# Optimization experiments

Hardware: AMD Instinct MI355X
Metric: run time of the kernel (lower is better)

## Reference

```python
import jax, jax.numpy as jnp
import numpy as np

B, SQ, SKV, D = 4, 4096, 4096, 64

def setup_inputs() -> dict:
    key = jax.random.key(0)
    kq, kv = jax.random.split(key)
    query = jax.random.normal(kq, (B, SQ, D), dtype=jnp.float32)
    value = jax.random.normal(kv, (B, SKV, D), dtype=jnp.float32)
    return {"query": query, "value": value}

def reference(query, value):
    # scores = Q @ V^T  (value acts as both keys and values; no 1/sqrt(d) scaling)
    scores = jnp.einsum('bqd,bkd->bqk', query, value)  # [B, SQ, SKV]
    dist = jax.nn.softmax(scores, axis=-1)
    context = jnp.einsum('bqk,bkd->bqd', dist, value)  # [B, SQ, D]
    return context
```

## Files before the change

kernel.cpp:

```cpp
#include <hip/hip_runtime.h>


#define NB   4
#define SQ   4096
#define SKV  4096
#define DH   64
#define L2E  1.44269504088896340736f

typedef _Float16 half8 __attribute__((ext_vector_type(8)));
typedef _Float16 half2v __attribute__((ext_vector_type(2)));
typedef __attribute__((ext_vector_type(4))) float f32x4;
typedef unsigned short u16;

__device__ __forceinline__ u16 f2h(float f) {
  _Float16 h = (_Float16)f;
  return __builtin_bit_cast(u16, h);
}

__global__ __launch_bounds__(256) void prep_kernel(
    const float* __restrict__ V, u16* __restrict__ vh, u16* __restrict__ vt) {
  __shared__ u16 ldsT[16 * 72];
  int blk = blockIdx.x;
  int b   = blk >> 8;
  int rem = blk & 255;
  int j0  = (rem >> 2) << 6;
  int d0  = (rem & 3) << 4;
  int t   = threadIdx.x;
  int j   = t >> 2;
  int dc  = (t & 3) << 2;

  const float* src = V + ((size_t)(b * SKV) + j0 + j) * DH + d0 + dc;
  float4 v4 = *(const float4*)src;
  u16 h[4] = {f2h(v4.x), f2h(v4.y), f2h(v4.z), f2h(v4.w)};
  unsigned p0 = (unsigned)h[0] | ((unsigned)h[1] << 16);
  unsigned p1 = (unsigned)h[2] | ((unsigned)h[3] << 16);
  size_t go = ((size_t)(b * SKV) + j0 + j) * DH + d0 + dc;
  *(uint2*)(vh + go) = make_uint2(p0, p1);

#pragma unroll
  for (int k = 0; k < 4; ++k) ldsT[(dc + k) * 72 + j] = h[k];
  __syncthreads();

  int dl = t >> 4;
  int jc = (t & 15) << 2;
  u16 tr[4];
#pragma unroll
  for (int k = 0; k < 4; ++k) tr[k] = ldsT[dl * 72 + jc + k];
  unsigned q0 = (unsigned)tr[0] | ((unsigned)tr[1] << 16);
  unsigned q1 = (unsigned)tr[2] | ((unsigned)tr[3] << 16);
  *(uint2*)(vt + ((size_t)(b * DH) + d0 + dl) * SKV + j0 + jc) = make_uint2(q0, q1);
}

__global__ __launch_bounds__(256, 4) void attn_kernel(
    const float* __restrict__ Q,
    const u16* __restrict__ vh,
    const u16* __restrict__ vt,
    u16* __restrict__ po,
    float* __restrict__ pm,
    float* __restrict__ pl,
    int S, int kvLen) {
  __shared__ __align__(16) u16 s_v[64 * 72];
  __shared__ __align__(16) u16 s_vt[64 * 72];
  __shared__ __align__(16) u16 s_pt[8][64 * 20];

  int blk  = blockIdx.x;
  int tile = blk / S;
  int s    = blk - tile * S;
  int b    = tile >> 5;
  int q0   = (tile & 31) << 7;
  int kv0  = s * kvLen;
  int t    = threadIdx.x;
  int wave = t >> 6;
  int lane = t & 63;
  int col  = lane & 15;
  int quad = lane >> 4;
  int qw   = q0 + (wave << 5);

  half8 qf[2][2];
#pragma unroll
  for (int set = 0; set < 2; ++set) {
#pragma unroll
    for (int kc = 0; kc < 2; ++kc) {
      const float* qp = Q + ((size_t)(b * SQ) + qw + set * 16 + col) * DH +
                        kc * 32 + (quad << 3);
      float4 a0 = *(const float4*)qp;
      float4 a1 = *(const float4*)(qp + 4);
      half8 h;
      h[0] = (_Float16)(a0.x * L2E); h[1] = (_Float16)(a0.y * L2E);
      h[2] = (_Float16)(a0.z * L2E); h[3] = (_Float16)(a0.w * L2E);
      h[4] = (_Float16)(a1.x * L2E); h[5] = (_Float16)(a1.y * L2E);
      h[6] = (_Float16)(a1.z * L2E); h[7] = (_Float16)(a1.w * L2E);
      qf[set][kc] = h;
    }
  }

  f32x4 o[2][4];
  float m_r[2][4], l_r[2][4];
#pragma unroll
  for (int set = 0; set < 2; ++set)
#pragma unroll
    for (int nf = 0; nf < 4; ++nf) {
      o[set][nf] = (f32x4){0.f, 0.f, 0.f, 0.f};
      m_r[set][nf] = -1e30f;
      l_r[set][nf] = 0.f;
    }

  int sr = t >> 2;
  int sc = (t & 3) << 4;
  const u16* gv  = vh + (size_t)(b * SKV) * DH;
  const u16* gvt = vt + (size_t)(b * DH) * SKV;

  for (int j0 = kv0; j0 < kv0 + kvLen; j0 += 64) {
    __syncthreads();
    {
      size_t g = (size_t)(j0 + sr) * DH + sc;
      uint4 a0 = *(const uint4*)(gv + g);
      uint4 a1 = *(const uint4*)(gv + g + 8);
      size_t gt = (size_t)sr * SKV + j0 + sc;
      uint4 c0 = *(const uint4*)(gvt + gt);
      uint4 c1 = *(const uint4*)(gvt + gt + 8);
      int l0 = sr * 72 + sc;
      *(uint4*)(s_v + l0)      = a0;
      *(uint4*)(s_v + l0 + 8)  = a1;
      *(uint4*)(s_vt + l0)     = c0;
      *(uint4*)(s_vt + l0 + 8) = c1;
    }
    __syncthreads();

    f32x4 sf[2][4];
#pragma unroll
    for (int set = 0; set < 2; ++set)
#pragma unroll
      for (int nf = 0; nf < 4; ++nf) sf[set][nf] = (f32x4){0.f, 0.f, 0.f, 0.f};
#pragma unroll
    for (int nf = 0; nf < 4; ++nf) {
#pragma unroll
      for (int kc = 0; kc < 2; ++kc) {
        half8 bv = *(const half8*)(s_v + (nf * 16 + col) * 72 + kc * 32 + (quad << 3));
        sf[0][nf] = __builtin_amdgcn_mfma_f32_16x16x32_f16(qf[0][kc], bv, sf[0][nf], 0, 0, 0);
        sf[1][nf] = __builtin_amdgcn_mfma_f32_16x16x32_f16(qf[1][kc], bv, sf[1][nf], 0, 0, 0);
      }
    }

#pragma unroll
    for (int set = 0; set < 2; ++set) {
      float tm[4];
#pragma unroll
      for (int r = 0; r < 4; ++r)
        tm[r] = fmaxf(fmaxf(sf[set][0][r], sf[set][1][r]),
                      fmaxf(sf[set][2][r], sf[set][3][r]));
      half2v h01 = {(_Float16)tm[0], (_Float16)tm[1]};
      half2v h23 = {(_Float16)tm[2], (_Float16)tm[3]};
#pragma unroll
      for (int mask = 1; mask <= 8; mask <<= 1) {
        int i01 = __shfl_xor(__builtin_bit_cast(int, h01), mask, 64);
        int i23 = __shfl_xor(__builtin_bit_cast(int, h23), mask, 64);
        h01 = __builtin_elementwise_max(h01, __builtin_bit_cast(half2v, i01));
        h23 = __builtin_elementwise_max(h23, __builtin_bit_cast(half2v, i23));
      }
      tm[0] = (float)h01[0]; tm[1] = (float)h01[1];
      tm[2] = (float)h23[0]; tm[3] = (float)h23[1];

      float al[4];
#pragma unroll
      for (int r = 0; r < 4; ++r) {
        float mn = fmaxf(m_r[set][r], tm[r]);
        al[r] = exp2f(m_r[set][r] - mn);
        m_r[set][r] = mn;
      }
      float rs[4] = {0.f, 0.f, 0.f, 0.f};
#pragma unroll
      for (int nf = 0; nf < 4; ++nf) {
#pragma unroll
        for (int r = 0; r < 4; ++r) {
          float p = exp2f(sf[set][nf][r] - m_r[set][r]);
          sf[set][nf][r] = p;
          rs[r] += p;
        }
      }
#pragma unroll
      for (int r = 0; r < 4; ++r) l_r[set][r] = l_r[set][r] * al[r] + rs[r];
#pragma unroll
      for (int nf = 0; nf < 4; ++nf)
#pragma unroll
        for (int r = 0; r < 4; ++r) o[set][nf][r] *= al[r];

      u16* pt = &s_pt[wave * 2 + set][0];
#pragma unroll
      for (int nf = 0; nf < 4; ++nf) {
        int j = nf * 16 + col;
        unsigned long long pk =
            (unsigned long long)f2h(sf[set][nf][0]) |
            ((unsigned long long)f2h(sf[set][nf][1]) << 16) |
            ((unsigned long long)f2h(sf[set][nf][2]) << 32) |
            ((unsigned long long)f2h(sf[set][nf][3]) << 48);
        *(unsigned long long*)(pt + j * 20 + (quad << 2)) = pk;
      }
    }

#pragma unroll
    for (int kc = 0; kc < 2; ++kc) {
      half8 pa0, pa1;
      const u16* pt0 = &s_pt[wave * 2 + 0][0];
      const u16* pt1 = &s_pt[wave * 2 + 1][0];
#pragma unroll
      for (int jj = 0; jj < 8; ++jj) {
        int k = kc * 32 + (quad << 3) + jj;
        pa0[jj] = __builtin_bit_cast(_Float16, pt0[k * 20 + col]);
        pa1[jj] = __builtin_bit_cast(_Float16, pt1[k * 20 + col]);
      }
#pragma unroll
      for (int nf = 0; nf < 4; ++nf) {
        half8 bw = *(const half8*)(s_vt + (nf * 16 + col) * 72 + kc * 32 + (quad << 3));
        o[0][nf] = __builtin_amdgcn_mfma_f32_16x16x32_f16(pa0, bw, o[0][nf], 0, 0, 0);
        o[1][nf] = __builtin_amdgcn_mfma_f32_16x16x32_f16(pa1, bw, o[1][nf], 0, 0, 0);
      }
    }
  }

#pragma unroll
  for (int set = 0; set < 2; ++set)
#pragma unroll
    for (int mask = 1; mask <= 8; mask <<= 1)
#pragma unroll
      for (int r = 0; r < 4; ++r)
        l_r[set][r] += __shfl_xor(l_r[set][r], mask, 64);

  int pidx = tile * S + s;
  u16* pob = po + (size_t)pidx * 128 * 64;
#pragma unroll
  for (int set = 0; set < 2; ++set) {
#pragma unroll
    for (int nf = 0; nf < 4; ++nf)
#pragma unroll
      for (int r = 0; r < 4; ++r) {
        int row = (wave << 5) + set * 16 + (quad << 2) + r;
        pob[row * 64 + nf * 16 + col] = f2h(o[set][nf][r]);
      }
  }
  if (col == 0) {
#pragma unroll
    for (int set = 0; set < 2; ++set)
#pragma unroll
      for (int r = 0; r < 4; ++r) {
        int row = (wave << 5) + set * 16 + (quad << 2) + r;
        pm[(size_t)pidx * 128 + row] = m_r[set][r];
        pl[(size_t)pidx * 128 + row] = l_r[set][r];
      }
  }
}

__global__ __launch_bounds__(256) void combine_kernel(
    const u16* __restrict__ po,
    const float* __restrict__ pm,
    const float* __restrict__ pl,
    float* __restrict__ out, int S) {
  int t    = threadIdx.x;
  int rowg = blockIdx.x * 32 + (t >> 3);
  int tile = rowg >> 7;
  int row  = rowg & 127;
  int dc   = (t & 7) << 3;

  float mv[8], lv[8];
  float M = -1e30f;
  for (int s = 0; s < S; ++s) {
    mv[s] = pm[(size_t)(tile * S + s) * 128 + row];
    lv[s] = pl[(size_t)(tile * S + s) * 128 + row];
    M = fmaxf(M, mv[s]);
  }
  float L = 0.f, w[8];
  for (int s = 0; s < S; ++s) {
    w[s] = exp2f(mv[s] - M);
    L += lv[s] * w[s];
  }
  float acc[8] = {0.f, 0.f, 0.f, 0.f, 0.f, 0.f, 0.f, 0.f};
  for (int s = 0; s < S; ++s) {
    const u16* p = po + (size_t)(tile * S + s) * 8192 + row * 64 + dc;
    uint4 raw = *(const uint4*)p;
    half8 x = __builtin_bit_cast(half8, raw);
#pragma unroll
    for (int k = 0; k < 8; ++k) acc[k] += w[s] * (float)x[k];
  }
  float invL = 1.0f / L;
  float* op = out + (size_t)rowg * 64 + dc;
  f32x4 o0 = (f32x4){acc[0], acc[1], acc[2], acc[3]};
  f32x4 o1 = (f32x4){acc[4], acc[5], acc[6], acc[7]};
  *(f32x4*)op       = o0 * invL;
  *(f32x4*)(op + 4) = o1 * invL;
}

extern "C" void kernel_launch(void* const* d_in, const int* in_sizes, int n_in,
                              void* d_out, int out_size, void* d_ws, size_t ws_size,
                              hipStream_t stream) {
  const float* Q = (const float*)d_in[0];
  const float* V = (const float*)d_in[1];
  float* out = (float*)d_out;

  const size_t convBytes = (size_t)2 * NB * SKV * DH * 2;
  auto partBytes = [](int S) {
    return (size_t)NB * 32 * S * ((size_t)128 * 64 * 2 + 128 * 8);
  };
  int S = 8;
  while (S > 1 && ws_size < convBytes + partBytes(S)) S >>= 1;
  int kvLen = SKV / S;

  u16* vh = (u16*)d_ws;
  u16* vt = vh + (size_t)NB * SKV * DH;
  u16* po = vt + (size_t)NB * SKV * DH;
  float* pm = (float*)(po + (size_t)NB * 32 * S * 128 * 64);
  float* pl = pm + (size_t)NB * 32 * S * 128;

  prep_kernel<<<NB * 256, 256, 0, stream>>>(V, vh, vt);
  attn_kernel<<<NB * 32 * S, 256, 0, stream>>>(Q, vh, vt, po, pm, pl, S, kvLen);
  combine_kernel<<<NB * SQ / 32, 256, 0, stream>>>(po, pm, pl, out, S);
}
```

Before: 119.0 us.

## Double-buffer V tiles and keep P in registers via transposed MFMA

Swaps the MFMA operand order so scores come out transposed (query rows along lanes). The softmax max and sum then need only two cross-lane shuffles, and P can feed the second matmul straight from registers through 16x16x16 MFMAs, with no LDS round-trip. V and V^T tiles are double-buffered in LDS with register prefetch, which drops one barrier per iteration. The epilogue stages the output through LDS for coalesced vector stores. The row max is now computed in fp32 instead of fp16, and P is converted with round-toward-zero packing.

```diff
diff --git a/kernel.cpp b/kernel.cpp
--- a/kernel.cpp
+++ b/kernel.cpp
@@ -8,13 +8,20 @@
 #define L2E  1.44269504088896340736f
 
 typedef _Float16 half8 __attribute__((ext_vector_type(8)));
+typedef _Float16 half4 __attribute__((ext_vector_type(4)));
 typedef _Float16 half2v __attribute__((ext_vector_type(2)));
-typedef __attribute__((ext_vector_type(4))) float f32x4;
+typedef float f32x4 __attribute__((ext_vector_type(4)));
 typedef unsigned short u16;
+
+#define MFMA16(a, b, c) __builtin_amdgcn_mfma_f32_16x16x16f16((a), (b), (c), 0, 0, 0)
+#define MFMA32(a, b, c) __builtin_amdgcn_mfma_f32_16x16x32_f16((a), (b), (c), 0, 0, 0)
 
 __device__ __forceinline__ u16 f2h(float f) {
   _Float16 h = (_Float16)f;
   return __builtin_bit_cast(u16, h);
+}
+__device__ __forceinline__ half2v pkrtz(float a, float b) {
+  return __builtin_bit_cast(half2v, __builtin_amdgcn_cvt_pkrtz(a, b));
 }
 
 __global__ __launch_bounds__(256) void prep_kernel(
@@ -59,9 +66,7 @@
     float* __restrict__ pm,
     float* __restrict__ pl,
     int S, int kvLen) {
-  __shared__ __align__(16) u16 s_v[64 * 72];
-  __shared__ __align__(16) u16 s_vt[64 * 72];
-  __shared__ __align__(16) u16 s_pt[8][64 * 20];
+  __shared__ __align__(16) u16 lds[2][2][64 * 72];
 
   int blk  = blockIdx.x;
   int tile = blk / S;
@@ -95,37 +100,46 @@
   }
 
   f32x4 o[2][4];
-  float m_r[2][4], l_r[2][4];
+  float m_r[2] = {-1e30f, -1e30f};
+  float l_r[2] = {0.f, 0.f};
 #pragma unroll
   for (int set = 0; set < 2; ++set)
 #pragma unroll
-    for (int nf = 0; nf < 4; ++nf) {
-      o[set][nf] = (f32x4){0.f, 0.f, 0.f, 0.f};
-      m_r[set][nf] = -1e30f;
-      l_r[set][nf] = 0.f;
-    }
+    for (int nf = 0; nf < 4; ++nf) o[set][nf] = (f32x4){0.f, 0.f, 0.f, 0.f};
 
   int sr = t >> 2;
   int sc = (t & 3) << 4;
   const u16* gv  = vh + (size_t)(b * SKV) * DH;
   const u16* gvt = vt + (size_t)(b * DH) * SKV;
-
-  for (int j0 = kv0; j0 < kv0 + kvLen; j0 += 64) {
+  int l0 = sr * 72 + sc;
+
+  {
+    size_t g  = (size_t)(kv0 + sr) * DH + sc;
+    size_t gt = (size_t)sr * SKV + kv0 + sc;
+    *(uint4*)(&lds[0][0][l0])     = *(const uint4*)(gv + g);
+    *(uint4*)(&lds[0][0][l0 + 8]) = *(const uint4*)(gv + g + 8);
+    *(uint4*)(&lds[0][1][l0])     = *(const uint4*)(gvt + gt);
+    *(uint4*)(&lds[0][1][l0 + 8]) = *(const uint4*)(gvt + gt + 8);
+  }
+
+  int nIter = kvLen >> 6;
+  int cur = 0;
+  for (int it = 0; it < nIter; ++it) {
     __syncthreads();
-    {
-      size_t g = (size_t)(j0 + sr) * DH + sc;
-      uint4 a0 = *(const uint4*)(gv + g);
-      uint4 a1 = *(const uint4*)(gv + g + 8);
+
+    uint4 a0, a1, c0, c1;
+    bool more = (it + 1) < nIter;
+    if (more) {
+      int j0 = kv0 + ((it + 1) << 6);
+      size_t g  = (size_t)(j0 + sr) * DH + sc;
       size_t gt = (size_t)sr * SKV + j0 + sc;
-      uint4 c0 = *(const uint4*)(gvt + gt);
-      uint4 c1 = *(const uint4*)(gvt + gt + 8);
-      int l0 = sr * 72 + sc;
-      *(uint4*)(s_v + l0)      = a0;
-      *(uint4*)(s_v + l0 + 8)  = a1;
-      *(uint4*)(s_vt + l0)     = c0;
-      *(uint4*)(s_vt + l0 + 8) = c1;
-    }
-    __syncthreads();
+      a0 = *(const uint4*)(gv + g);
+      a1 = *(const uint4*)(gv + g + 8);
+      c0 = *(const uint4*)(gvt + gt);
+      c1 = *(const uint4*)(gvt + gt + 8);
+    }
+    const u16* sv  = &lds[cur][0][0];
+    const u16* svt = &lds[cur][1][0];
 
     f32x4 sf[2][4];
 #pragma unroll
@@ -136,117 +150,108 @@
     for (int nf = 0; nf < 4; ++nf) {
 #pragma unroll
       for (int kc = 0; kc < 2; ++kc) {
-        half8 bv = *(const half8*)(s_v + (nf * 16 + col) * 72 + kc * 32 + (quad << 3));
-        sf[0][nf] = __builtin_amdgcn_mfma_f32_16x16x32_f16(qf[0][kc], bv, sf[0][nf], 0, 0, 0);
-        sf[1][nf] = __builtin_amdgcn_mfma_f32_16x16x32_f16(qf[1][kc], bv, sf[1][nf], 0, 0, 0);
+        half8 av = *(const half8*)(sv + (nf * 16 + col) * 72 + kc * 32 + (quad << 3));
+        sf[0][nf] = MFMA32(av, qf[0][kc], sf[0][nf]);
+        sf[1][nf] = MFMA32(av, qf[1][kc], sf[1][nf]);
       }
     }
 
+    half4 pf[2][4];
 #pragma unroll
     for (int set = 0; set < 2; ++set) {
-      float tm[4];
-#pragma unroll
-      for (int r = 0; r < 4; ++r)
-        tm[r] = fmaxf(fmaxf(sf[set][0][r], sf[set][1][r]),
-                      fmaxf(sf[set][2][r], sf[set][3][r]));
-      half2v h01 = {(_Float16)tm[0], (_Float16)tm[1]};
-      half2v h23 = {(_Float16)tm[2], (_Float16)tm[3]};
-#pragma unroll
-      for (int mask = 1; mask <= 8; mask <<= 1) {
-        int i01 = __shfl_xor(__builtin_bit_cast(int, h01), mask, 64);
-        int i23 = __shfl_xor(__builtin_bit_cast(int, h23), mask, 64);
-        h01 = __builtin_elementwise_max(h01, __builtin_bit_cast(half2v, i01));
-        h23 = __builtin_elementwise_max(h23, __builtin_bit_cast(half2v, i23));
+      float tm = sf[set][0][0];
+#pragma unroll
+      for (int nf = 0; nf < 4; ++nf)
+#pragma unroll
+        for (int r = 0; r < 4; ++r) tm = fmaxf(tm, sf[set][nf][r]);
+      tm = fmaxf(tm, __shfl_xor(tm, 16, 64));
+      tm = fmaxf(tm, __shfl_xor(tm, 32, 64));
+      float mn = fmaxf(m_r[set], tm);
+      float al = exp2f(m_r[set] - mn);
+      m_r[set] = mn;
+      float rs = 0.f;
+#pragma unroll
+      for (int nf = 0; nf < 4; ++nf) {
+        float p0 = exp2f(sf[set][nf][0] - mn);
+        float p1 = exp2f(sf[set][nf][1] - mn);
+        float p2 = exp2f(sf[set][nf][2] - mn);
+        float p3 = exp2f(sf[set][nf][3] - mn);
+        rs += (p0 + p1) + (p2 + p3);
+        half2v lo = pkrtz(p0, p1);
+        half2v hi = pkrtz(p2, p3);
+        pf[set][nf] = __builtin_shufflevector(lo, hi, 0, 1, 2, 3);
       }
-      tm[0] = (float)h01[0]; tm[1] = (float)h01[1];
-      tm[2] = (float)h23[0]; tm[3] = (float)h23[1];
-
-      float al[4];
-#pragma unroll
-      for (int r = 0; r < 4; ++r) {
-        float mn = fmaxf(m_r[set][r], tm[r]);
-        al[r] = exp2f(m_r[set][r] - mn);
-        m_r[set][r] = mn;
+      l_r[set] = l_r[set] * al + rs;
+#pragma unroll
+      for (int nf = 0; nf < 4; ++nf)
+#pragma unroll
+        for (int r = 0; r < 4; ++r) o[set][nf][r] *= al;
+    }
+
+#pragma unroll
+    for (int kc4 = 0; kc4 < 4; ++kc4) {
+#pragma unroll
+      for (int nf2 = 0; nf2 < 4; ++nf2) {
+        half4 avt = *(const half4*)(svt + (nf2 * 16 + col) * 72 + kc4 * 16 + (quad << 2));
+        o[0][nf2] = MFMA16(avt, pf[0][kc4], o[0][nf2]);
+        o[1][nf2] = MFMA16(avt, pf[1][kc4], o[1][nf2]);
       }
-      float rs[4] = {0.f, 0.f, 0.f, 0.f};
-#pragma unroll
-      for (int nf = 0; nf < 4; ++nf) {
-#pragma unroll
-        for (int r = 0; r < 4; ++r) {
-          float p = exp2f(sf[set][nf][r] - m_r[set][r]);
-          sf[set][nf][r] = p;
-          rs[r] += p;
-        }
+    }
+
+    if (more) {
+      u16* dv  = &lds[cur ^ 1][0][0];
+      u16* dvt = &lds[cur ^ 1][1][0];
+      *(uint4*)(dv + l0)      = a0;
+      *(uint4*)(dv + l0 + 8)  = a1;
+      *(uint4*)(dvt + l0)     = c0;
+      *(uint4*)(dvt + l0 + 8) = c1;
+    }
+    cur ^= 1;
+  }
+
+#pragma unroll
+  for (int set = 0; set < 2; ++set) {
+    l_r[set] += __shfl_xor(l_r[set], 16, 64);
+    l_r[set] += __shfl_xor(l_r[set], 32, 64);
+  }
+  int pidx = tile * S + s;
+  if (quad == 0) {
+#pragma unroll
+    for (int set = 0; set < 2; ++set) {
+      int row = (wave << 5) + set * 16 + col;
+      pm[(size_t)pidx * 128 + row] = m_r[set];
+      pl[(size_t)pidx * 128 + row] = l_r[set];
+    }
+  }
+
+  __syncthreads();
+  u16* tp = &lds[0][0][0];
+#pragma unroll
+  for (int set = 0; set < 2; ++set) {
+    int q = (wave << 5) + set * 16 + col;
+#pragma unroll
+    for (int nf2 = 0; nf2 < 4; ++nf2) {
+#pragma unroll
+      for (int r2 = 0; r2 < 4; r2 += 2) {
+        unsigned pk = (unsigned)f2h(o[set][nf2][r2]) |
+                      ((unsigned)f2h(o[set][nf2][r2 + 1]) << 16);
+        int d = nf2 * 16 + (quad << 2) + r2;
+        *(unsigned*)(tp + q * 72 + d) = pk;
       }
-#pragma unroll
-      for (int r = 0; r < 4; ++r) l_r[set][r] = l_r[set][r] * al[r] + rs[r];
-#pragma unroll
-      for (int nf = 0; nf < 4; ++nf)
-#pragma unroll
-        for (int r = 0; r < 4; ++r) o[set][nf][r] *= al[r];
-
-      u16* pt = &s_pt[wave * 2 + set][0];
-#pragma unroll
-      for (int nf = 0; nf < 4; ++nf) {
-        int j = nf * 16 + col;
-        unsigned long long pk =
-            (unsigned long long)f2h(sf[set][nf][0]) |
-            ((unsigned long long)f2h(sf[set][nf][1]) << 16) |
-            ((unsigned long long)f2h(sf[set][nf][2]) << 32) |
-            ((unsigned long long)f2h(sf[set][nf][3]) << 48);
-        *(unsigned long long*)(pt + j * 20 + (quad << 2)) = pk;
-      }
-    }
-
-#pragma unroll
-    for (int kc = 0; kc < 2; ++kc) {
-      half8 pa0, pa1;
-      const u16* pt0 = &s_pt[wave * 2 + 0][0];
-      const u16* pt1 = &s_pt[wave * 2 + 1][0];
-#pragma unroll
-      for (int jj = 0; jj < 8; ++jj) {
-        int k = kc * 32 + (quad << 3) + jj;
-        pa0[jj] = __builtin_bit_cast(_Float16, pt0[k * 20 + col]);
-        pa1[jj] = __builtin_bit_cast(_Float16, pt1[k * 20 + col]);
-      }
-#pragma unroll
-      for (int nf = 0; nf < 4; ++nf) {
-        half8 bw = *(const half8*)(s_vt + (nf * 16 + col) * 72 + kc * 32 + (quad << 3));
-        o[0][nf] = __builtin_amdgcn_mfma_f32_16x16x32_f16(pa0, bw, o[0][nf], 0, 0, 0);
-        o[1][nf] = __builtin_amdgcn_mfma_f32_16x16x32_f16(pa1, bw, o[1][nf], 0, 0, 0);
-      }
-    }
-  }
-
-#pragma unroll
-  for (int set = 0; set < 2; ++set)
-#pragma unroll
-    for (int mask = 1; mask <= 8; mask <<= 1)
-#pragma unroll
-      for (int r = 0; r < 4; ++r)
-        l_r[set][r] += __shfl_xor(l_r[set][r], mask, 64);
-
-  int pidx = tile * S + s;
-  u16* pob = po + (size_t)pidx * 128 * 64;
-#pragma unroll
-  for (int set = 0; set < 2; ++set) {
-#pragma unroll
-    for (int nf = 0; nf < 4; ++nf)
-#pragma unroll
-      for (int r = 0; r < 4; ++r) {
-        int row = (wave << 5) + set * 16 + (quad << 2) + r;
-        pob[row * 64 + nf * 16 + col] = f2h(o[set][nf][r]);
-      }
-  }
-  if (col == 0) {
-#pragma unroll
-    for (int set = 0; set < 2; ++set)
-#pragma unroll
-      for (int r = 0; r < 4; ++r) {
-        int row = (wave << 5) + set * 16 + (quad << 2) + r;
-        pm[(size_t)pidx * 128 + row] = m_r[set][r];
-        pl[(size_t)pidx * 128 + row] = l_r[set][r];
-      }
+    }
+  }
+  __syncthreads();
+  {
+    u16* pob = po + (size_t)pidx * 128 * 64;
+    int q = t >> 1, hc = (t & 1) << 5;
+    uint4 x0 = *(const uint4*)(tp + q * 72 + hc);
+    uint4 x1 = *(const uint4*)(tp + q * 72 + hc + 8);
+    uint4 x2 = *(const uint4*)(tp + q * 72 + hc + 16);
+    uint4 x3 = *(const uint4*)(tp + q * 72 + hc + 24);
+    *(uint4*)(pob + q * 64 + hc)      = x0;
+    *(uint4*)(pob + q * 64 + hc + 8)  = x1;
+    *(uint4*)(pob + q * 64 + hc + 16) = x2;
+    *(uint4*)(pob + q * 64 + hc + 24) = x3;
   }
 }
 
```

After: 127.7 us. 1.07x slower.
